# Kernel optimization log

Measured on AMD Instinct MI355X. Metric: run time of the kernel, lower is better.

The kernel has to match this reference:

```python
import jax, jax.numpy as jnp
import numpy as np

N_HEAD = 32
N_KV_HEAD = 8
HD = 64  # head dim
N_EMBD = 2048
B, T = 2, 2048
ROPE_THETA = 10000.0


def _apply_rope(x, cos, sin):
    # x: [B, T, H, HD]; cos/sin: [T, HD//2]. Interleaved complex pairs (even, odd),
    # matching torch.view_as_complex on x.reshape(..., -1, 2).
    x0 = x[..., 0::2]
    x1 = x[..., 1::2]
    c = cos[None, :, None, :]
    s = sin[None, :, None, :]
    o0 = x0 * c - x1 * s
    o1 = x0 * s + x1 * c
    return jnp.stack([o0, o1], axis=-1).reshape(x.shape)


def setup_inputs() -> dict:
    key = jax.random.key(0)
    k1, k2, k3 = jax.random.split(key, 3)
    x = jax.random.normal(k1, (B, T, N_EMBD), dtype=jnp.float32)
    Wqkv = jax.random.normal(k2, ((N_HEAD + 2 * N_KV_HEAD) * HD, N_EMBD), dtype=jnp.float32) * 0.02
    Wproj = jax.random.normal(k3, (N_EMBD, N_EMBD), dtype=jnp.float32) * 0.02
    # precompute_freqs_cis as in llm.c (llama path)
    freqs = 1.0 / (ROPE_THETA ** (np.arange(0, HD, 2, dtype=np.float32) / HD))
    ang = np.outer(np.arange(T, dtype=np.float32), freqs)  # [T, HD//2]
    freqs_cos = jnp.asarray(np.cos(ang), dtype=jnp.float32)
    freqs_sin = jnp.asarray(np.sin(ang), dtype=jnp.float32)
    return {"x": x, "Wqkv": Wqkv, "Wproj": Wproj,
            "freqs_cos": freqs_cos, "freqs_sin": freqs_sin, "start_pos": -1}


def reference(x, Wqkv, Wproj, freqs_cos, freqs_sin, start_pos):
    Bx, Tx, C = x.shape
    n_rep = N_HEAD // N_KV_HEAD
    qkv = x @ Wqkv.T  # [B, T, (H + 2*KV)*HD]
    q = qkv[..., : N_HEAD * HD].reshape(Bx, Tx, N_HEAD, HD)
    k = qkv[..., N_HEAD * HD: (N_HEAD + N_KV_HEAD) * HD].reshape(Bx, Tx, N_KV_HEAD, HD)
    v = qkv[..., (N_HEAD + N_KV_HEAD) * HD:].reshape(Bx, Tx, N_KV_HEAD, HD)
    # RoPE on q, k
    q = _apply_rope(q, freqs_cos, freqs_sin)
    k = _apply_rope(k, freqs_cos, freqs_sin)
    # start_pos < 0: training path, no KV cache. GQA repeat of kv heads.
    k = jnp.repeat(k, n_rep, axis=2)  # [B, T, H, HD]
    v = jnp.repeat(v, n_rep, axis=2)
    q = q.transpose(0, 2, 1, 3)  # [B, H, T, HD]
    k = k.transpose(0, 2, 1, 3)
    v = v.transpose(0, 2, 1, 3)
    scale = 1.0 / np.sqrt(HD).astype(np.float32)
    scores = jnp.einsum("bhtd,bhsd->bhts", q, k) * scale  # [B, H, T, T]
    causal = jnp.tril(jnp.ones((Tx, Tx), dtype=bool))
    scores = jnp.where(causal[None, None, :, :], scores, -jnp.inf)
    att = jax.nn.softmax(scores.astype(jnp.float32), axis=-1).astype(q.dtype)
    y = jnp.einsum("bhts,bhsd->bhtd", att, v)
    y = y.transpose(0, 2, 1, 3).reshape(Bx, Tx, C)
    return y @ Wproj.T
```

## Files before the change

kernel.cpp:

```cpp
#include <hip/hip_runtime.h>
#include <hip/hip_bf16.h>
#include <cstdint>

#define NH   32
#define NKV  8
#define HD   64
#define CE   2048
#define BB   2
#define TT   2048
#define QKVD 3072
#define MM   (BB*TT)

typedef float  f32x4  __attribute__((ext_vector_type(4)));
typedef float  f32x16 __attribute__((ext_vector_type(16)));
typedef short  s16x8  __attribute__((ext_vector_type(8)));
typedef unsigned short u16;

#define AS1 __attribute__((address_space(1)))
#define AS3 __attribute__((address_space(3)))
#define GLDS16(src, dst) __builtin_amdgcn_global_load_lds( \
    (const AS1 uint32_t*)(src), (AS3 uint32_t*)(dst), 16, 0, 0)

static __device__ __forceinline__ float bf2f(u16 u) {
    union { uint32_t u; float f; } v; v.u = ((uint32_t)u) << 16; return v.f;
}
static __device__ __forceinline__ u16 f2bf(float f) {
    union { float f; uint32_t u; } v; v.f = f;
    uint32_t r = v.u + 0x7fffu + ((v.u >> 16) & 1u);
    return (u16)(r >> 16);
}
static __device__ __forceinline__ uint32_t cvtpk(float lo, float hi) {
    uint32_t r;
    asm("v_cvt_pk_bf16_f32 %0, %1, %2" : "=v"(r) : "v"(lo), "v"(hi));
    return r;
}
static __device__ __forceinline__ void plswap(uint32_t &a, uint32_t &b) {
    asm volatile("v_permlane32_swap_b32 %0, %1" : "+v"(a), "+v"(b));
}

__global__ void k_f32_to_bf16(const float* __restrict__ in, uint32_t* __restrict__ out, int n8) {
    int i = blockIdx.x * blockDim.x + threadIdx.x;
    if (i >= n8) return;
    const float4* p = reinterpret_cast<const float4*>(in) + (size_t)i * 2;
    float4 a = p[0], b = p[1];
    uint4 o;
    o.x = cvtpk(a.x, a.y); o.y = cvtpk(a.z, a.w);
    o.z = cvtpk(b.x, b.y); o.w = cvtpk(b.z, b.w);
    *reinterpret_cast<uint4*>(out + (size_t)i * 4) = o;
}

__global__ __launch_bounds__(256) void k_gemm_qkv(const u16* __restrict__ A,
                                                  const u16* __restrict__ Bm,
                                                  u16* __restrict__ Qb,
                                                  u16* __restrict__ Kb,
                                                  u16* __restrict__ Vt,
                                                  const float* __restrict__ fcos,
                                                  const float* __restrict__ fsin) {
    __shared__ u16 As[128 * 32];
    __shared__ u16 Bs[128 * 32];
    const int K = CE;
    const int c  = blockIdx.x + 24 * blockIdx.y;
    const int nc = (c & 7) * 96 + (c >> 3);
    const int m0 = (nc / 24) * 128;
    const int n0 = (nc % 24) * 128;

    const int tid  = threadIdx.x;
    const int w    = tid >> 6;
    const int lane = tid & 63;
    const int lr   = lane & 15, lg = lane >> 4;
    const int wm   = (w >> 1) * 64, wn = (w & 1) * 64;

    const int o0 = w * 2048 + lane * 16, o1 = o0 + 1024;
    const int ar0 = o0 >> 6, ar1 = o1 >> 6;
    const int ac0 = (o0 & 63) >> 1, ac1 = (o1 & 63) >> 1;
    const size_t aof0 = (size_t)(m0 + ar0) * K + ac0;
    const size_t aof1 = (size_t)(m0 + ar1) * K + ac1;
    const size_t bof0 = (size_t)(n0 + ar0) * K + ac0;
    const size_t bof1 = (size_t)(n0 + ar1) * K + ac1;
    u16* dA0 = &As[w * 1024];       u16* dA1 = &As[w * 1024 + 512];
    u16* dB0 = &Bs[w * 1024];       u16* dB1 = &Bs[w * 1024 + 512];

    f32x4 acc[4][4] = {};

    for (int k0 = 0; k0 < K; k0 += 32) {
        GLDS16(A  + aof0 + k0, dA0);
        GLDS16(A  + aof1 + k0, dA1);
        GLDS16(Bm + bof0 + k0, dB0);
        GLDS16(Bm + bof1 + k0, dB1);
        __syncthreads();
        s16x8 af[4], bf[4];
        #pragma unroll
        for (int i = 0; i < 4; ++i)
            af[i] = *reinterpret_cast<const s16x8*>(&As[(wm + i * 16 + lr) * 32 + lg * 8]);
        #pragma unroll
        for (int j = 0; j < 4; ++j)
            bf[j] = *reinterpret_cast<const s16x8*>(&Bs[(wn + j * 16 + lr) * 32 + lg * 8]);
        #pragma unroll
        for (int i = 0; i < 4; ++i)
            #pragma unroll
            for (int j = 0; j < 4; ++j)
                acc[i][j] = __builtin_amdgcn_mfma_f32_16x16x32_bf16(af[i], bf[j], acc[i][j], 0, 0, 0);
        __syncthreads();
    }

    const float QS = 0.18033688011112042f;
    const int bb = m0 / TT;
    const int tb = m0 - bb * TT + wm;
    #pragma unroll
    for (int i = 0; i < 4; ++i) {
        const int t0 = tb + i * 16 + lg * 4;
        #pragma unroll
        for (int j = 0; j < 4; ++j) {
            const int n = n0 + wn + j * 16 + lr;
            if (n0 < NH * HD) {
                const int hh = n >> 6, d = n & 63;
                #pragma unroll
                for (int r = 0; r < 4; ++r) {
                    const int t = t0 + r;
                    const float cc = fcos[t * 32 + (d >> 1)];
                    const float ss = fsin[t * 32 + (d >> 1)];
                    float v = acc[i][j][r];
                    float p = __shfl_xor(v, 1, 64);
                    float o = ((lr & 1) ? (p * ss + v * cc) : (v * cc - p * ss)) * QS;
                    float po = __shfl_xor(o, 1, 64);
                    if (!(lr & 1))
                        *reinterpret_cast<uint32_t*>(Qb + ((size_t)((bb * NH + hh) * TT + t)) * HD + d) = cvtpk(o, po);
                }
            } else if (n0 < (NH + NKV) * HD) {
                const int fk = n - NH * HD;
                const int hh = fk >> 6, d = fk & 63;
                #pragma unroll
                for (int r = 0; r < 4; ++r) {
                    const int t = t0 + r;
                    const float cc = fcos[t * 32 + (d >> 1)];
                    const float ss = fsin[t * 32 + (d >> 1)];
                    float v = acc[i][j][r];
                    float p = __shfl_xor(v, 1, 64);
                    float o = (lr & 1) ? (p * ss + v * cc) : (v * cc - p * ss);
                    float po = __shfl_xor(o, 1, 64);
                    if (!(lr & 1))
                        *reinterpret_cast<uint32_t*>(Kb + ((size_t)((bb * NKV + hh) * TT + t)) * HD + d) = cvtpk(o, po);
                }
            } else {
                const int fv = n - (NH + NKV) * HD;
                const int vh = fv >> 6, d = fv & 63;
                uint2 st;
                st.x = cvtpk(acc[i][j][0], acc[i][j][1]);
                st.y = cvtpk(acc[i][j][2], acc[i][j][3]);
                *reinterpret_cast<uint2*>(Vt + ((size_t)(bb * NKV + vh) * HD + d) * TT + t0) = st;
            }
        }
    }
}

__global__ __launch_bounds__(256) void k_gemm_bt(const u16* __restrict__ A,
                                                 const u16* __restrict__ Bm,
                                                 float* __restrict__ Cout,
                                                 int M, int N, int K) {
    __shared__ u16 As[128 * 32];
    __shared__ u16 Bs[128 * 32];
    const int c  = blockIdx.x + 16 * blockIdx.y;
    const int nc = (c & 7) * 64 + (c >> 3);
    const int m0 = (nc >> 4) * 128;
    const int n0 = (nc & 15) * 128;

    const int tid  = threadIdx.x;
    const int w    = tid >> 6;
    const int lane = tid & 63;
    const int lr   = lane & 15, lg = lane >> 4;
    const int wm   = (w >> 1) * 64, wn = (w & 1) * 64;

    const int o0 = w * 2048 + lane * 16, o1 = o0 + 1024;
    const int ar0 = o0 >> 6, ar1 = o1 >> 6;
    const int ac0 = (o0 & 63) >> 1, ac1 = (o1 & 63) >> 1;
    const size_t aof0 = (size_t)(m0 + ar0) * K + ac0;
    const size_t aof1 = (size_t)(m0 + ar1) * K + ac1;
    const size_t bof0 = (size_t)(n0 + ar0) * K + ac0;
    const size_t bof1 = (size_t)(n0 + ar1) * K + ac1;
    u16* dA0 = &As[w * 1024];       u16* dA1 = &As[w * 1024 + 512];
    u16* dB0 = &Bs[w * 1024];       u16* dB1 = &Bs[w * 1024 + 512];

    f32x4 acc[4][4] = {};

    for (int k0 = 0; k0 < K; k0 += 32) {
        GLDS16(A  + aof0 + k0, dA0);
        GLDS16(A  + aof1 + k0, dA1);
        GLDS16(Bm + bof0 + k0, dB0);
        GLDS16(Bm + bof1 + k0, dB1);
        __syncthreads();
        s16x8 af[4], bf[4];
        #pragma unroll
        for (int i = 0; i < 4; ++i)
            af[i] = *reinterpret_cast<const s16x8*>(&As[(wm + i * 16 + lr) * 32 + lg * 8]);
        #pragma unroll
        for (int j = 0; j < 4; ++j)
            bf[j] = *reinterpret_cast<const s16x8*>(&Bs[(wn + j * 16 + lr) * 32 + lg * 8]);
        #pragma unroll
        for (int i = 0; i < 4; ++i)
            #pragma unroll
            for (int j = 0; j < 4; ++j)
                acc[i][j] = __builtin_amdgcn_mfma_f32_16x16x32_bf16(af[i], bf[j], acc[i][j], 0, 0, 0);
        __syncthreads();
    }

    #pragma unroll
    for (int i = 0; i < 4; ++i)
        #pragma unroll
        for (int j = 0; j < 4; ++j)
            #pragma unroll
            for (int r = 0; r < 4; ++r) {
                int m = m0 + wm + i * 16 + lg * 4 + r;
                int n = n0 + wn + j * 16 + lr;
                Cout[(size_t)m * N + n] = acc[i][j][r];
            }
}

__global__ __launch_bounds__(256) void k_attn(const u16* __restrict__ Q,
                                              const u16* __restrict__ Kb,
                                              const u16* __restrict__ Vt,
                                              u16* __restrict__ Y) {
    __shared__ u16 Ks[2][4096];
    __shared__ u16 Vs[2][4096];

    const int tid = threadIdx.x;
    const int w = tid >> 6, lane = tid & 63;
    const int ql = lane & 31, hi = lane >> 5;
    const int hi16 = hi << 4;
    const int b = blockIdx.z, h = blockIdx.y, kvh = h >> 2;

    const u16* qbase = Q  + ((size_t)(b * NH  + h  ) * TT) * HD;
    const u16* kbase = Kb + ((size_t)(b * NKV + kvh) * TT) * HD;
    const u16* vbase = Vt + ((size_t)(b * NKV + kvh) * HD) * TT;

    const int o0 = w * 2048 + lane * 16, o1 = o0 + 1024;
    const int r0 = o0 >> 7, r1 = o1 >> 7;
    const int c0 = (o0 & 127) ^ ((r0 & 7) << 4);
    const int c1 = (o1 & 127) ^ ((r1 & 7) << 4);
    const size_t kof0 = (size_t)r0 * HD + (c0 >> 1);
    const size_t kof1 = (size_t)r1 * HD + (c1 >> 1);
    const size_t vof0 = (size_t)r0 * TT + (c0 >> 1);
    const size_t vof1 = (size_t)r1 * TT + (c1 >> 1);

    const char* KsB = (const char*)&Ks[0][0];
    const char* VsB = (const char*)&Vs[0][0];
    const int krb0 = (0 * 32 + ql) * 128, ksz0 = ((0 * 32 + ql) & 7) << 4;
    const int krb1 = (1 * 32 + ql) * 128, ksz1 = ((1 * 32 + ql) & 7) << 4;

    #pragma unroll 1
    for (int pi = 0; pi < 2; ++pi) {
        const int j    = pi ? (int)blockIdx.x : (15 - (int)blockIdx.x);
        const int q0w  = j * 128 + w * 32;
        const int nt   = 2 * j + 2;
        const int tmxw = (q0w + 31) >> 6;
        const int qabs = q0w + ql;

        s16x8 qf[4];
        #pragma unroll
        for (int ds = 0; ds < 4; ++ds)
            qf[ds] = *reinterpret_cast<const s16x8*>(qbase + (size_t)qabs * HD + ds * 16 + 8 * hi);
        asm volatile("s_waitcnt vmcnt(0)" ::: "memory");

        GLDS16(kbase + kof0, &Ks[0][w * 1024]);
        GLDS16(kbase + kof1, &Ks[0][w * 1024 + 512]);
        GLDS16(vbase + vof0, &Vs[0][w * 1024]);
        GLDS16(vbase + vof1, &Vs[0][w * 1024 + 512]);

        float mrow = -1e30f, lrowp = 0.f;
        f32x16 oT0 = {}, oT1 = {};

        for (int t = 0; t < nt; ++t) {
            const int cur = t & 1;
            const int kv0 = t * 64;
            if (t + 1 < nt) {
                const size_t kb2 = (size_t)(kv0 + 64) * HD;
                GLDS16(kbase + kb2 + kof0, &Ks[cur ^ 1][w * 1024]);
                GLDS16(kbase + kb2 + kof1, &Ks[cur ^ 1][w * 1024 + 512]);
                GLDS16(vbase + (kv0 + 64) + vof0, &Vs[cur ^ 1][w * 1024]);
                GLDS16(vbase + (kv0 + 64) + vof1, &Vs[cur ^ 1][w * 1024 + 512]);
                asm volatile("s_waitcnt vmcnt(4)" ::: "memory");
            } else {
                asm volatile("s_waitcnt vmcnt(0)" ::: "memory");
            }
            __builtin_amdgcn_s_barrier();
            __builtin_amdgcn_sched_barrier(0);

            if (t <= tmxw) {
                const int bufo = cur * 8192;

                f32x16 sc0 = {}, sc1 = {};
                __builtin_amdgcn_s_setprio(1);
                #pragma unroll
                for (int ds = 0; ds < 4; ++ds) {
                    s16x8 k0 = *reinterpret_cast<const s16x8*>(KsB + bufo + krb0 + (((ds << 5) | hi16) ^ ksz0));
                    s16x8 k1 = *reinterpret_cast<const s16x8*>(KsB + bufo + krb1 + (((ds << 5) | hi16) ^ ksz1));
                    sc0 = __builtin_amdgcn_mfma_f32_32x32x16_bf16(k0, qf[ds], sc0, 0, 0, 0);
                    sc1 = __builtin_amdgcn_mfma_f32_32x32x16_bf16(k1, qf[ds], sc1, 0, 0, 0);
                }
                __builtin_amdgcn_s_setprio(0);

                float p0[16], p1[16];
                #pragma unroll
                for (int r = 0; r < 16; ++r) { p0[r] = sc0[r]; p1[r] = sc1[r]; }

                if (t == tmxw) {
                    const int dq = qabs - kv0 - 4 * hi;
                    #pragma unroll
                    for (int r = 0; r < 16; ++r) {
                        const int kr = (r & 3) + 8 * (r >> 2);
                        p0[r] = (kr      <= dq) ? p0[r] : -1e30f;
                        p1[r] = (kr + 32 <= dq) ? p1[r] : -1e30f;
                    }
                }

                float tmax = fmaxf(p0[0], p1[0]);
                #pragma unroll
                for (int r = 1; r < 16; ++r) tmax = fmaxf(tmax, fmaxf(p0[r], p1[r]));
                if (__any(tmax > mrow + 8.f)) {
                    float tf = fmaxf(tmax, __shfl_xor(tmax, 32, 64));
                    float mn = fmaxf(mrow, tf);
                    float alpha = __builtin_amdgcn_exp2f(mrow - mn);
                    mrow = mn;
                    lrowp *= alpha;
                    #pragma unroll
                    for (int r = 0; r < 16; ++r) { oT0[r] *= alpha; oT1[r] *= alpha; }
                }

                float sum = 0.f;
                #pragma unroll
                for (int r = 0; r < 16; ++r) {
                    p0[r] = __builtin_amdgcn_exp2f(p0[r] - mrow);
                    p1[r] = __builtin_amdgcn_exp2f(p1[r] - mrow);
                    sum += p0[r] + p1[r];
                }
                lrowp += sum;

                __builtin_amdgcn_s_setprio(1);
                #pragma unroll
                for (int ks = 0; ks < 2; ++ks) {
                    uint32_t a0 = cvtpk(p0[ks * 8 + 0], p0[ks * 8 + 1]);
                    uint32_t b0 = cvtpk(p0[ks * 8 + 4], p0[ks * 8 + 5]);
                    plswap(a0, b0);
                    uint32_t a1 = cvtpk(p0[ks * 8 + 2], p0[ks * 8 + 3]);
                    uint32_t b1 = cvtpk(p0[ks * 8 + 6], p0[ks * 8 + 7]);
                    plswap(a1, b1);
                    union { uint32_t d[4]; s16x8 v; } pb;
                    pb.d[0] = a0; pb.d[1] = a1; pb.d[2] = b0; pb.d[3] = b1;
                    const int colb = (0 << 6) | (ks << 5) | hi16;
                    s16x8 v0 = *reinterpret_cast<const s16x8*>(VsB + bufo + krb0 + (colb ^ ksz0));
                    s16x8 v1 = *reinterpret_cast<const s16x8*>(VsB + bufo + krb1 + (colb ^ ksz1));
                    oT0 = __builtin_amdgcn_mfma_f32_32x32x16_bf16(v0, pb.v, oT0, 0, 0, 0);
                    oT1 = __builtin_amdgcn_mfma_f32_32x32x16_bf16(v1, pb.v, oT1, 0, 0, 0);
                }
                #pragma unroll
                for (int ks = 0; ks < 2; ++ks) {
                    uint32_t a0 = cvtpk(p1[ks * 8 + 0], p1[ks * 8 + 1]);
                    uint32_t b0 = cvtpk(p1[ks * 8 + 4], p1[ks * 8 + 5]);
                    plswap(a0, b0);
                    uint32_t a1 = cvtpk(p1[ks * 8 + 2], p1[ks * 8 + 3]);
                    uint32_t b1 = cvtpk(p1[ks * 8 + 6], p1[ks * 8 + 7]);
                    plswap(a1, b1);
                    union { uint32_t d[4]; s16x8 v; } pb;
                    pb.d[0] = a0; pb.d[1] = a1; pb.d[2] = b0; pb.d[3] = b1;
                    const int colb = (1 << 6) | (ks << 5) | hi16;
                    s16x8 v0 = *reinterpret_cast<const s16x8*>(VsB + bufo + krb0 + (colb ^ ksz0));
                    s16x8 v1 = *reinterpret_cast<const s16x8*>(VsB + bufo + krb1 + (colb ^ ksz1));
                    oT0 = __builtin_amdgcn_mfma_f32_32x32x16_bf16(v0, pb.v, oT0, 0, 0, 0);
                    oT1 = __builtin_amdgcn_mfma_f32_32x32x16_bf16(v1, pb.v, oT1, 0, 0, 0);
                }
                __builtin_amdgcn_s_setprio(0);
            }

            __builtin_amdgcn_sched_barrier(0);
            __builtin_amdgcn_s_barrier();
        }

        lrowp += __shfl_xor(lrowp, 32, 64);
        const float rinv = 1.f / lrowp;
        const size_t yrow = ((size_t)(b * TT + qabs) * NH + h) * HD;
        #pragma unroll
        for (int rp = 0; rp < 8; ++rp) {
            const int d = ((2 * rp) & 3) + 8 * (rp >> 1) + 4 * hi;
            *reinterpret_cast<uint32_t*>(Y + yrow + d) =
                cvtpk(oT0[2 * rp] * rinv, oT0[2 * rp + 1] * rinv);
            *reinterpret_cast<uint32_t*>(Y + yrow + 32 + d) =
                cvtpk(oT1[2 * rp] * rinv, oT1[2 * rp + 1] * rinv);
        }
    }
}

extern "C" void kernel_launch(void* const* d_in, const int* in_sizes, int n_in,
                              void* d_out, int out_size, void* d_ws, size_t ws_size,
                              hipStream_t stream) {
    (void)in_sizes; (void)n_in; (void)out_size; (void)ws_size;
    const float* x     = (const float*)d_in[0];
    const float* wqkv  = (const float*)d_in[1];
    const float* wproj = (const float*)d_in[2];
    const float* fcos  = (const float*)d_in[3];
    const float* fsin  = (const float*)d_in[4];

    char* ws = (char*)d_ws;
    size_t off = 0;
    auto alloc = [&](size_t bytes) { void* p = ws + off; off += (bytes + 255) & ~(size_t)255; return p; };
    u16* Xbf  = (u16*)alloc((size_t)MM * CE * 2);
    u16* Wqb  = (u16*)alloc((size_t)QKVD * CE * 2);
    u16* Wpb  = (u16*)alloc((size_t)CE * CE * 2);
    u16* Qb   = (u16*)alloc((size_t)BB * NH * TT * HD * 2);
    u16* Kbuf = (u16*)alloc((size_t)BB * NKV * TT * HD * 2);
    u16* Vtb  = (u16*)alloc((size_t)BB * NKV * HD * TT * 2);
    u16* Yb   = (u16*)alloc((size_t)MM * CE * 2);

    k_f32_to_bf16<<<(MM * CE / 8 + 255) / 256, 256, 0, stream>>>(x, (uint32_t*)Xbf, MM * CE / 8);
    k_f32_to_bf16<<<(QKVD * CE / 8 + 255) / 256, 256, 0, stream>>>(wqkv, (uint32_t*)Wqb, QKVD * CE / 8);
    k_f32_to_bf16<<<(CE * CE / 8 + 255) / 256, 256, 0, stream>>>(wproj, (uint32_t*)Wpb, CE * CE / 8);

    dim3 g1(QKVD / 128, MM / 128);
    k_gemm_qkv<<<g1, 256, 0, stream>>>(Xbf, Wqb, Qb, Kbuf, Vtb, fcos, fsin);

    dim3 ga(8, NH, BB);
    k_attn<<<ga, 256, 0, stream>>>(Qb, Kbuf, Vtb, Yb);

    dim3 g2(CE / 128, MM / 128);
    k_gemm_bt<<<g2, 256, 0, stream>>>(Yb, Wpb, (float*)d_out, MM, CE, CE);
}
```

Before: 215.4 us.

## Transpose QK MFMA output so RoPE pairs land in one lane

For Q/K tiles the MFMA operands are swapped, so each lane holds four consecutive head-dim values for one token. RoPE can then be applied in registers without cross-lane shuffles, and each lane writes 8-byte stores. A small prepass interleaves cos/sin into a [d/2][T] float2 table so the epilogue gets coalesced loads. The cost is one extra kernel launch and a small workspace buffer. The attention max reduction is also reordered slightly.

```diff
diff --git a/kernel.cpp b/kernel.cpp
--- a/kernel.cpp
+++ b/kernel.cpp
@@ -49,13 +49,21 @@
     *reinterpret_cast<uint4*>(out + (size_t)i * 4) = o;
 }
 
+__global__ void k_build_cs(const float* __restrict__ fcos, const float* __restrict__ fsin,
+                           float2* __restrict__ csT) {
+    int i = blockIdx.x * blockDim.x + threadIdx.x;
+    if (i >= 32 * TT) return;
+    int d2 = i >> 11, t = i & (TT - 1);
+    float2 cs; cs.x = fcos[t * 32 + d2]; cs.y = fsin[t * 32 + d2];
+    csT[i] = cs;
+}
+
 __global__ __launch_bounds__(256) void k_gemm_qkv(const u16* __restrict__ A,
                                                   const u16* __restrict__ Bm,
                                                   u16* __restrict__ Qb,
                                                   u16* __restrict__ Kb,
                                                   u16* __restrict__ Vt,
-                                                  const float* __restrict__ fcos,
-                                                  const float* __restrict__ fsin) {
+                                                  const float2* __restrict__ csT) {
     __shared__ u16 As[128 * 32];
     __shared__ u16 Bs[128 * 32];
     const int K = CE;
@@ -80,6 +88,8 @@
     u16* dA0 = &As[w * 1024];       u16* dA1 = &As[w * 1024 + 512];
     u16* dB0 = &Bs[w * 1024];       u16* dB1 = &Bs[w * 1024 + 512];
 
+    const bool isqk = (n0 < (NH + NKV) * HD);
+
     f32x4 acc[4][4] = {};
 
     for (int k0 = 0; k0 < K; k0 += 32) {
@@ -95,53 +105,65 @@
         #pragma unroll
         for (int j = 0; j < 4; ++j)
             bf[j] = *reinterpret_cast<const s16x8*>(&Bs[(wn + j * 16 + lr) * 32 + lg * 8]);
-        #pragma unroll
-        for (int i = 0; i < 4; ++i)
-            #pragma unroll
-            for (int j = 0; j < 4; ++j)
-                acc[i][j] = __builtin_amdgcn_mfma_f32_16x16x32_bf16(af[i], bf[j], acc[i][j], 0, 0, 0);
+        if (isqk) {
+            #pragma unroll
+            for (int i = 0; i < 4; ++i)
+                #pragma unroll
+                for (int j = 0; j < 4; ++j)
+                    acc[i][j] = __builtin_amdgcn_mfma_f32_16x16x32_bf16(bf[j], af[i], acc[i][j], 0, 0, 0);
+        } else {
+            #pragma unroll
+            for (int i = 0; i < 4; ++i)
+                #pragma unroll
+                for (int j = 0; j < 4; ++j)
+                    acc[i][j] = __builtin_amdgcn_mfma_f32_16x16x32_bf16(af[i], bf[j], acc[i][j], 0, 0, 0);
+        }
         __syncthreads();
     }
 
     const float QS = 0.18033688011112042f;
     const int bb = m0 / TT;
     const int tb = m0 - bb * TT + wm;
-    #pragma unroll
-    for (int i = 0; i < 4; ++i) {
-        const int t0 = tb + i * 16 + lg * 4;
-        #pragma unroll
-        for (int j = 0; j < 4; ++j) {
-            const int n = n0 + wn + j * 16 + lr;
-            if (n0 < NH * HD) {
-                const int hh = n >> 6, d = n & 63;
-                #pragma unroll
-                for (int r = 0; r < 4; ++r) {
-                    const int t = t0 + r;
-                    const float cc = fcos[t * 32 + (d >> 1)];
-                    const float ss = fsin[t * 32 + (d >> 1)];
-                    float v = acc[i][j][r];
-                    float p = __shfl_xor(v, 1, 64);
-                    float o = ((lr & 1) ? (p * ss + v * cc) : (v * cc - p * ss)) * QS;
-                    float po = __shfl_xor(o, 1, 64);
-                    if (!(lr & 1))
-                        *reinterpret_cast<uint32_t*>(Qb + ((size_t)((bb * NH + hh) * TT + t)) * HD + d) = cvtpk(o, po);
-                }
-            } else if (n0 < (NH + NKV) * HD) {
-                const int fk = n - NH * HD;
-                const int hh = fk >> 6, d = fk & 63;
-                #pragma unroll
-                for (int r = 0; r < 4; ++r) {
-                    const int t = t0 + r;
-                    const float cc = fcos[t * 32 + (d >> 1)];
-                    const float ss = fsin[t * 32 + (d >> 1)];
-                    float v = acc[i][j][r];
-                    float p = __shfl_xor(v, 1, 64);
-                    float o = (lr & 1) ? (p * ss + v * cc) : (v * cc - p * ss);
-                    float po = __shfl_xor(o, 1, 64);
-                    if (!(lr & 1))
-                        *reinterpret_cast<uint32_t*>(Kb + ((size_t)((bb * NKV + hh) * TT + t)) * HD + d) = cvtpk(o, po);
-                }
-            } else {
+    if (isqk) {
+        const bool isq = (n0 < NH * HD);
+        #pragma unroll
+        for (int i = 0; i < 4; ++i) {
+            const int t = tb + i * 16 + lr;
+            #pragma unroll
+            for (int j = 0; j < 4; ++j) {
+                const int nb = n0 + wn + j * 16 + 4 * lg;
+                const int d  = nb & 63;
+                const int d2 = d >> 1;
+                const float2 cs0 = csT[d2 * TT + t];
+                const float2 cs1 = csT[(d2 + 1) * TT + t];
+                float x0 = acc[i][j][0], x1 = acc[i][j][1];
+                float x2 = acc[i][j][2], x3 = acc[i][j][3];
+                float e0 = x0 * cs0.x - x1 * cs0.y;
+                float e1 = x0 * cs0.y + x1 * cs0.x;
+                float e2 = x2 * cs1.x - x3 * cs1.y;
+                float e3 = x2 * cs1.y + x3 * cs1.x;
+                uint2 st;
+                u16* base;
+                if (isq) {
+                    st.x = cvtpk(e0 * QS, e1 * QS);
+                    st.y = cvtpk(e2 * QS, e3 * QS);
+                    base = Qb + ((size_t)((bb * NH + (nb >> 6)) * TT + t)) * HD + d;
+                } else {
+                    st.x = cvtpk(e0, e1);
+                    st.y = cvtpk(e2, e3);
+                    const int fk = nb - NH * HD;
+                    base = Kb + ((size_t)((bb * NKV + (fk >> 6)) * TT + t)) * HD + d;
+                }
+                *reinterpret_cast<uint2*>(base) = st;
+            }
+        }
+    } else {
+        #pragma unroll
+        for (int i = 0; i < 4; ++i) {
+            const int t0 = tb + i * 16 + lg * 4;
+            #pragma unroll
+            for (int j = 0; j < 4; ++j) {
+                const int n = n0 + wn + j * 16 + lr;
                 const int fv = n - (NH + NKV) * HD;
                 const int vh = fv >> 6, d = fv & 63;
                 uint2 st;
@@ -314,7 +336,7 @@
 
                 float tmax = fmaxf(p0[0], p1[0]);
                 #pragma unroll
-                for (int r = 1; r < 16; ++r) tmax = fmaxf(tmax, fmaxf(p0[r], p1[r]));
+                for (int r = 1; r < 16; ++r) tmax = fmaxf(fmaxf(tmax, p0[r]), p1[r]);
                 if (__any(tmax > mrow + 8.f)) {
                     float tf = fmaxf(tmax, __shfl_xor(tmax, 32, 64));
                     float mn = fmaxf(mrow, tf);
@@ -401,20 +423,22 @@
     char* ws = (char*)d_ws;
     size_t off = 0;
     auto alloc = [&](size_t bytes) { void* p = ws + off; off += (bytes + 255) & ~(size_t)255; return p; };
-    u16* Xbf  = (u16*)alloc((size_t)MM * CE * 2);
-    u16* Wqb  = (u16*)alloc((size_t)QKVD * CE * 2);
-    u16* Wpb  = (u16*)alloc((size_t)CE * CE * 2);
-    u16* Qb   = (u16*)alloc((size_t)BB * NH * TT * HD * 2);
-    u16* Kbuf = (u16*)alloc((size_t)BB * NKV * TT * HD * 2);
-    u16* Vtb  = (u16*)alloc((size_t)BB * NKV * HD * TT * 2);
-    u16* Yb   = (u16*)alloc((size_t)MM * CE * 2);
+    u16*    Xbf  = (u16*)alloc((size_t)MM * CE * 2);
+    u16*    Wqb  = (u16*)alloc((size_t)QKVD * CE * 2);
+    u16*    Wpb  = (u16*)alloc((size_t)CE * CE * 2);
+    u16*    Qb   = (u16*)alloc((size_t)BB * NH * TT * HD * 2);
+    u16*    Kbuf = (u16*)alloc((size_t)BB * NKV * TT * HD * 2);
+    u16*    Vtb  = (u16*)alloc((size_t)BB * NKV * HD * TT * 2);
+    u16*    Yb   = (u16*)alloc((size_t)MM * CE * 2);
+    float2* csT  = (float2*)alloc((size_t)32 * TT * sizeof(float2));
 
     k_f32_to_bf16<<<(MM * CE / 8 + 255) / 256, 256, 0, stream>>>(x, (uint32_t*)Xbf, MM * CE / 8);
     k_f32_to_bf16<<<(QKVD * CE / 8 + 255) / 256, 256, 0, stream>>>(wqkv, (uint32_t*)Wqb, QKVD * CE / 8);
     k_f32_to_bf16<<<(CE * CE / 8 + 255) / 256, 256, 0, stream>>>(wproj, (uint32_t*)Wpb, CE * CE / 8);
+    k_build_cs<<<(32 * TT + 255) / 256, 256, 0, stream>>>(fcos, fsin, csT);
 
     dim3 g1(QKVD / 128, MM / 128);
-    k_gemm_qkv<<<g1, 256, 0, stream>>>(Xbf, Wqb, Qb, Kbuf, Vtb, fcos, fsin);
+    k_gemm_qkv<<<g1, 256, 0, stream>>>(Xbf, Wqb, Qb, Kbuf, Vtb, csT);
 
     dim3 ga(8, NH, BB);
     k_attn<<<ga, 256, 0, stream>>>(Qb, Kbuf, Vtb, Yb);
```

Result: slower. 235.6 us (+9.4%).
